# Optimization experiments

Hardware: AMD Instinct MI355X
Metric: run time of the kernel (lower is better)

The kernel has to match this reference:

```python
import jax, jax.numpy as jnp
import numpy as np

B, NN, K, F = 256, 90, 10, 90  # graphs, nodes/graph, retain_node, node_len
TENDENCY = 0.7


def setup_inputs() -> dict:
    key = jax.random.key(0)
    ks = jax.random.split(key, 16)
    N = B * NN
    # fully-connected (no self-loop) edge list per graph, block-offset per graph
    a = np.repeat(np.arange(NN), NN)
    b = np.tile(np.arange(NN), NN)
    m = a != b
    src0, dst0 = a[m], b[m]                      # [8010]
    off = (np.arange(B) * NN)[:, None]
    src = (src0[None, :] + off).ravel()
    dst = (dst0[None, :] + off).ravel()
    edge_index = jnp.asarray(np.stack([src, dst]), dtype=jnp.int64)
    E = edge_index.shape[1]
    batch = jnp.asarray(np.repeat(np.arange(B), NN), dtype=jnp.int64)
    s = 1.0 / np.sqrt(F)
    return {
        "x": jax.random.normal(ks[0], (N, F), jnp.float32),
        "edge_index": edge_index,
        "edge_attr": jax.random.uniform(ks[1], (E,), jnp.float32),
        "batch": batch,
        "W1r": jax.random.normal(ks[2], (F, F), jnp.float32) * s,
        "W1m": jax.random.normal(ks[3], (F, F), jnp.float32) * s,
        "b1": jnp.zeros((F,), jnp.float32),
        "W2r": jax.random.normal(ks[4], (F, F), jnp.float32) * s,
        "W2m": jax.random.normal(ks[5], (F, F), jnp.float32) * s,
        "b2": jnp.zeros((F,), jnp.float32),
        "pool_p": jax.random.normal(ks[6], (F,), jnp.float32),
        "lin_W": jax.random.normal(ks[7], (K * F, 2 * K * F + 1), jnp.float32) / np.sqrt(K * F),
        "lin_b": jnp.zeros((2 * K * F + 1,), jnp.float32),
        "cls_W": jax.random.normal(ks[8], (2 * K * F + 1, 1), jnp.float32) / np.sqrt(2 * K * F + 1),
        "cls_b": jnp.zeros((1,), jnp.float32),
    }


def reference(x, edge_index, edge_attr, batch, W1r, W1m, b1, W2r, W2m, b2,
              pool_p, lin_W, lin_b, cls_W, cls_b):
    src, dst = edge_index[0], edge_index[1]
    N = x.shape[0]

    def conv(h, Wr, Wm, b):  # edge-conditioned message passing
        msg = (h[src] @ Wm) * edge_attr[:, None]          # [E, F]
        agg = jax.ops.segment_sum(msg, dst, num_segments=N)
        return jax.nn.relu(h @ Wr + agg + b)

    def bn(h):  # fresh BatchNorm1d (gamma=1, beta=0), training-mode batch stats
        mu = h.mean(axis=0)
        var = h.var(axis=0)
        return (h - mu) * jax.lax.rsqrt(var + 1e-5)

    x = bn(conv(x, W1r, W1m, b1))
    x = bn(conv(x, W2r, W2m, b2))

    # category-aware top-k pooling: projection score, keep K nodes per graph
    score = TENDENCY * jnp.tanh((x @ pool_p) / jnp.linalg.norm(pool_p))  # [N]
    vals, idx = jax.lax.top_k(score.reshape(B, NN), K)                   # [B, K]
    xb = x.reshape(B, NN, F)
    xs = jnp.take_along_axis(xb, idx[:, :, None], axis=1) * vals[:, :, None]
    perm = (idx + (jnp.arange(B) * NN)[:, None]).reshape(-1)             # global node ids

    h = xs.reshape(B, K * F)
    h = h @ lin_W + lin_b
    out = jax.nn.sigmoid((h @ cls_W + cls_b).reshape(-1))                # [B]
    return (out, perm)
```

## Files before the change

kernel.cpp:

```cpp
#include <hip/hip_runtime.h>
#include <math.h>

#define NG   90
#define PD   96
#define STRD 100
#define KK   10
#define NB   256
#define NTOT (NB*NG)
#define EPG  8010
#define ARR  (PD*STRD)
#define SM_FLOATS (4*ARR)

__global__ __launch_bounds__(512, 2)
void layer_kernel(const float* __restrict__ xin,
                  const float* __restrict__ psIn, int apply_bn,
                  const float* __restrict__ attr,
                  const float* __restrict__ Wm, const float* __restrict__ Wr,
                  const float* __restrict__ bias,
                  float* __restrict__ hout, float* __restrict__ psOut,
                  int do_prep,
                  const float* __restrict__ linW, const float* __restrict__ linb,
                  const float* __restrict__ clsW, const float* __restrict__ clsb,
                  const float* __restrict__ poolp,
                  float* __restrict__ vlin, float* __restrict__ scal)
{
    extern __shared__ float sm[];
    float* s0  = sm;
    float* sA  = s0 + ARR;
    float* sWm = sA + ARR;
    float* sWr = sWm + ARR;
    __shared__ float sSum[96], sSq[96], sMu[96], sRs[96], sStat[192];

    const int g = blockIdx.x, tid = threadIdx.x;
    const int lane = tid & 63, wave = tid >> 6;
    const int cg = tid & 15;
    const int rg = tid >> 4;
    const int r0 = rg * 3;

    if (apply_bn) {
        if (tid < 192) {
            float s = 0.f;
            const float* p = psIn + tid;
#pragma unroll 8
            for (int b = 0; b < NB; b++) s += p[b * 192];
            sStat[tid] = s;
        }
        __syncthreads();
        if (tid < 96) {
            float m = sStat[tid] * (1.f / NTOT);
            float v = sStat[96 + tid] * (1.f / NTOT) - m * m;
            sMu[tid] = m; sRs[tid] = rsqrtf(v + 1e-5f);
        }
    } else if (tid < 96) { sMu[tid] = 0.f; sRs[tid] = 1.f; }
    if (tid < 96) { sSum[tid] = 0.f; sSq[tid] = 0.f; }
    __syncthreads();

    for (int idx = tid; idx < PD * PD; idx += 512) {
        int r = idx / PD, k = idx - (idx / PD) * PD;
        float v = 0.f;
        if (r < NG && k < NG) v = (xin[(size_t)(g * NG + r) * NG + k] - sMu[k]) * sRs[k];
        s0[r * STRD + k] = v;
    }
    for (int idx = tid; idx < PD * PD; idx += 512) {
        int s = idx / PD, d = idx - (idx / PD) * PD;
        float v = 0.f;
        if (s < NG && d < NG && d != s) v = attr[(size_t)g * EPG + s * 89 + (d > s ? d - 1 : d)];
        sA[d * STRD + s] = v;
    }
    for (int idx = tid; idx < PD * PD; idx += 512) {
        int k = idx / PD, c = idx - (idx / PD) * PD;
        bool ok = (k < NG && c < NG);
        sWm[c * STRD + k] = ok ? Wm[k * NG + c] : 0.f;
        sWr[c * STRD + k] = ok ? Wr[k * NG + c] : 0.f;
    }
    __syncthreads();

    float accM[3][6], accR[3][6];
#pragma unroll
    for (int i = 0; i < 3; i++)
#pragma unroll
        for (int j = 0; j < 6; j++) { accM[i][j] = 0.f; accR[i][j] = 0.f; }
    {
        const float* pX = s0 + r0 * STRD;
#pragma unroll 2
        for (int k = 0; k < PD; k += 4) {
            float4 xv[3], wm[6], wr[6];
#pragma unroll
            for (int i = 0; i < 3; i++) xv[i] = *(const float4*)(pX + i * STRD + k);
#pragma unroll
            for (int j = 0; j < 6; j++) {
                const int c = cg + 16 * j;
                wm[j] = *(const float4*)(sWm + c * STRD + k);
                wr[j] = *(const float4*)(sWr + c * STRD + k);
            }
#pragma unroll
            for (int i = 0; i < 3; i++)
#pragma unroll
                for (int j = 0; j < 6; j++) {
                    accM[i][j] = fmaf(xv[i].x, wm[j].x, accM[i][j]);
                    accM[i][j] = fmaf(xv[i].y, wm[j].y, accM[i][j]);
                    accM[i][j] = fmaf(xv[i].z, wm[j].z, accM[i][j]);
                    accM[i][j] = fmaf(xv[i].w, wm[j].w, accM[i][j]);
                    accR[i][j] = fmaf(xv[i].x, wr[j].x, accR[i][j]);
                    accR[i][j] = fmaf(xv[i].y, wr[j].y, accR[i][j]);
                    accR[i][j] = fmaf(xv[i].z, wr[j].z, accR[i][j]);
                    accR[i][j] = fmaf(xv[i].w, wr[j].w, accR[i][j]);
                }
        }
    }
    __syncthreads();

#pragma unroll
    for (int j = 0; j < 6; j++)
#pragma unroll
        for (int i = 0; i < 3; i++)
            s0[(cg + 16 * j) * STRD + (r0 + i)] = accM[i][j];
    __syncthreads();

    float h[3][6];
#pragma unroll
    for (int j = 0; j < 6; j++) {
        const int c = cg + 16 * j;
        float bj = (c < NG) ? bias[c] : 0.f;
#pragma unroll
        for (int i = 0; i < 3; i++) h[i][j] = accR[i][j] + bj;
    }
    {
        const float* pA = sA + r0 * STRD;
#pragma unroll 2
        for (int k = 0; k < PD; k += 4) {
            float4 av[3], mv[6];
#pragma unroll
            for (int i = 0; i < 3; i++) av[i] = *(const float4*)(pA + i * STRD + k);
#pragma unroll
            for (int j = 0; j < 6; j++) mv[j] = *(const float4*)(s0 + (cg + 16 * j) * STRD + k);
#pragma unroll
            for (int i = 0; i < 3; i++)
#pragma unroll
                for (int j = 0; j < 6; j++) {
                    h[i][j] = fmaf(av[i].x, mv[j].x, h[i][j]);
                    h[i][j] = fmaf(av[i].y, mv[j].y, h[i][j]);
                    h[i][j] = fmaf(av[i].z, mv[j].z, h[i][j]);
                    h[i][j] = fmaf(av[i].w, mv[j].w, h[i][j]);
                }
        }
    }

    float cs[6], cq[6];
#pragma unroll
    for (int j = 0; j < 6; j++) { cs[j] = 0.f; cq[j] = 0.f; }
#pragma unroll
    for (int i = 0; i < 3; i++) {
        int r = r0 + i;
        if (r < NG) {
#pragma unroll
            for (int j = 0; j < 6; j++) {
                int c = cg + 16 * j;
                if (c < NG) {
                    float v = fmaxf(h[i][j], 0.f);
                    hout[(size_t)(g * NG + r) * NG + c] = v;
                    cs[j] += v; cq[j] += v * v;
                }
            }
        }
    }
#pragma unroll
    for (int m = 16; m < 64; m <<= 1) {
#pragma unroll
        for (int j = 0; j < 6; j++) {
            cs[j] += __shfl_xor(cs[j], m);
            cq[j] += __shfl_xor(cq[j], m);
        }
    }
    if ((lane >> 4) == 0) {
#pragma unroll
        for (int j = 0; j < 6; j++) {
            int c = cg + 16 * j;
            if (c < NG) { atomicAdd(&sSum[c], cs[j]); atomicAdd(&sSq[c], cq[j]); }
        }
    }
    __syncthreads();
    if (tid < 96) psOut[g * 192 + tid] = sSum[tid];
    else if (tid < 192) psOut[g * 192 + tid] = sSq[tid - 96];

    if (do_prep) {
        if (wave < 4) {
            int row = g + 256 * wave;
            if (row < 900) {
                const float* rw = linW + (size_t)row * 1801;
                float acc = 0.f;
                for (int c2 = lane; c2 < 1801; c2 += 64) acc += rw[c2] * clsW[c2];
                for (int off = 32; off; off >>= 1) acc += __shfl_down(acc, off);
                if (lane == 0) vlin[row] = acc;
            }
        } else if (g == 0 && wave == 4) {
            float acc = 0.f;
            for (int c2 = lane; c2 < 1801; c2 += 64) acc += linb[c2] * clsW[c2];
            for (int off = 32; off; off >>= 1) acc += __shfl_down(acc, off);
            if (lane == 0) scal[0] = acc + clsb[0];
        } else if (g == 0 && wave == 5) {
            float acc = 0.f;
            for (int c2 = lane; c2 < NG; c2 += 64) acc += poolp[c2] * poolp[c2];
            for (int off = 32; off; off >>= 1) acc += __shfl_down(acc, off);
            if (lane == 0) scal[1] = rsqrtf(acc);
        }
    }
}

__global__ __launch_bounds__(256)
void final_kernel(const float* __restrict__ h2, const float* __restrict__ psIn,
                  const float* __restrict__ poolp,
                  const float* __restrict__ vlin, const float* __restrict__ scal,
                  float* __restrict__ out)
{
    __shared__ float sXN[NG * 91];
    __shared__ float sMu[96], sRs[96], sP[96], sStat[192];
    __shared__ float sScore[NG];
    __shared__ int   sIdx[KK];
    __shared__ float sVal[KK];
    __shared__ float sRed[4];
    const int g = blockIdx.x, tid = threadIdx.x;

    if (tid < 192) {
        float s = 0.f;
        const float* p = psIn + tid;
#pragma unroll 8
        for (int b = 0; b < NB; b++) s += p[b * 192];
        sStat[tid] = s;
    }
    __syncthreads();
    if (tid < NG) {
        float m = sStat[tid] * (1.f / NTOT);
        float v = sStat[96 + tid] * (1.f / NTOT) - m * m;
        sMu[tid] = m; sRs[tid] = rsqrtf(v + 1e-5f);
        sP[tid] = poolp[tid];
    }
    __syncthreads();

    const float* hg = h2 + (size_t)g * (NG * NG);
    for (int idx = tid; idx < NG * NG; idx += 256) {
        int d = idx / NG, f = idx - (idx / NG) * NG;
        sXN[d * 91 + f] = (hg[idx] - sMu[f]) * sRs[f];
    }
    __syncthreads();

    if (tid < NG) {
        float s = 0.f;
        for (int f = 0; f < NG; f++) s += sXN[tid * 91 + f] * sP[f];
        sScore[tid] = 0.7f * tanhf(s * scal[1]);
    }
    __syncthreads();

    if (tid < 64) {
        float va = sScore[tid];
        float vb = (tid + 64 < NG) ? sScore[tid + 64] : -1e30f;
        int ia = tid, ib = tid + 64;
        for (int k = 0; k < KK; k++) {
            float v; int i;
            if (va >= vb) { v = va; i = ia; } else { v = vb; i = ib; }
            for (int off = 1; off < 64; off <<= 1) {
                float v2 = __shfl_xor(v, off);
                int   i2 = __shfl_xor(i, off);
                if (v2 > v || (v2 == v && i2 < i)) { v = v2; i = i2; }
            }
            if (tid == 0) { sIdx[k] = i; sVal[k] = v; }
            if (i == ia) va = -1e30f;
            if (i == ib) vb = -1e30f;
        }
    }
    __syncthreads();

    if (tid < KK) out[NB + g * KK + tid] = (float)(g * NG + sIdx[tid]);

    float acc = 0.f;
    for (int j = tid; j < KK * NG; j += 256) {
        int k = j / NG, f = j - (j / NG) * NG;
        acc += sXN[sIdx[k] * 91 + f] * sVal[k] * vlin[j];
    }
    for (int off = 32; off; off >>= 1) acc += __shfl_down(acc, off);
    if ((tid & 63) == 0) sRed[tid >> 6] = acc;
    __syncthreads();
    if (tid == 0) {
        float tot = sRed[0] + sRed[1] + sRed[2] + sRed[3] + scal[0];
        out[g] = 1.f / (1.f + expf(-tot));
    }
}

extern "C" void kernel_launch(void* const* d_in, const int* in_sizes, int n_in,
                              void* d_out, int out_size, void* d_ws, size_t ws_size,
                              hipStream_t stream) {
    const float* x    = (const float*)d_in[0];
    const float* attr = (const float*)d_in[2];
    const float* W1r  = (const float*)d_in[4];
    const float* W1m  = (const float*)d_in[5];
    const float* b1   = (const float*)d_in[6];
    const float* W2r  = (const float*)d_in[7];
    const float* W2m  = (const float*)d_in[8];
    const float* b2   = (const float*)d_in[9];
    const float* poolp= (const float*)d_in[10];
    const float* linW = (const float*)d_in[11];
    const float* linb = (const float*)d_in[12];
    const float* clsW = (const float*)d_in[13];
    const float* clsb = (const float*)d_in[14];

    float* ws   = (float*)d_ws;
    float* ps1  = ws;
    float* ps2  = ps1 + NB * 192;
    float* vlin = ps2 + NB * 192;
    float* scal = vlin + 900;
    float* h1   = scal + 62;
    float* h2   = h1 + (size_t)NTOT * NG;

    const size_t smem = SM_FLOATS * sizeof(float);
    hipFuncSetAttribute((const void*)layer_kernel, hipFuncAttributeMaxDynamicSharedMemorySize, (int)smem);

    layer_kernel<<<NB, 512, smem, stream>>>(x,  nullptr, 0, attr, W1m, W1r, b1, h1, ps1,
                                            1, linW, linb, clsW, clsb, poolp, vlin, scal);
    layer_kernel<<<NB, 512, smem, stream>>>(h1, ps1, 1, attr, W2m, W2r, b2, h2, ps2,
                                            0, linW, linb, clsW, clsb, poolp, vlin, scal);
    final_kernel<<<NB, 256, 0, stream>>>(h2, ps2, poolp, vlin, scal, (float*)d_out);
}
```

Baseline: 234.4 us.

## Double threads per block with 3x3 register tiles and double-buffered LDS loads

Launches the layer kernel with 1024 threads per block instead of 512. Each thread now computes a 3x3 output tile, with waves arranged in a 4x4 grid over the 96x96 padded matrix, instead of a 3x6 tile. Both inner matmul loops are rewritten with software double-buffering of float4 shared-memory loads. The intent is more waves to hide latency and lower register pressure per thread. The trade-off is lower arithmetic intensity per LDS load, since each thread reuses fewer loaded values, plus a tighter launch-bounds register budget.

```diff
diff --git a/kernel.cpp b/kernel.cpp
--- a/kernel.cpp
+++ b/kernel.cpp
@@ -11,7 +11,7 @@
 #define ARR  (PD*STRD)
 #define SM_FLOATS (4*ARR)
 
-__global__ __launch_bounds__(512, 2)
+__global__ __launch_bounds__(1024, 4)
 void layer_kernel(const float* __restrict__ xin,
                   const float* __restrict__ psIn, int apply_bn,
                   const float* __restrict__ attr,
@@ -33,9 +33,9 @@
 
     const int g = blockIdx.x, tid = threadIdx.x;
     const int lane = tid & 63, wave = tid >> 6;
-    const int cg = tid & 15;
-    const int rg = tid >> 4;
-    const int r0 = rg * 3;
+    const int lr = lane >> 3, lc = lane & 7;
+    const int r0 = (wave >> 2) * 24 + lr * 3;
+    const int c0 = (wave & 3) * 24 + lc * 3;
 
     if (apply_bn) {
         if (tid < 192) {
@@ -55,19 +55,19 @@
     if (tid < 96) { sSum[tid] = 0.f; sSq[tid] = 0.f; }
     __syncthreads();
 
-    for (int idx = tid; idx < PD * PD; idx += 512) {
+    for (int idx = tid; idx < PD * PD; idx += 1024) {
         int r = idx / PD, k = idx - (idx / PD) * PD;
         float v = 0.f;
         if (r < NG && k < NG) v = (xin[(size_t)(g * NG + r) * NG + k] - sMu[k]) * sRs[k];
         s0[r * STRD + k] = v;
     }
-    for (int idx = tid; idx < PD * PD; idx += 512) {
+    for (int idx = tid; idx < PD * PD; idx += 1024) {
         int s = idx / PD, d = idx - (idx / PD) * PD;
         float v = 0.f;
         if (s < NG && d < NG && d != s) v = attr[(size_t)g * EPG + s * 89 + (d > s ? d - 1 : d)];
         sA[d * STRD + s] = v;
     }
-    for (int idx = tid; idx < PD * PD; idx += 512) {
+    for (int idx = tid; idx < PD * PD; idx += 1024) {
         int k = idx / PD, c = idx - (idx / PD) * PD;
         bool ok = (k < NG && c < NG);
         sWm[c * STRD + k] = ok ? Wm[k * NG + c] : 0.f;
@@ -75,87 +75,172 @@
     }
     __syncthreads();
 
-    float accM[3][6], accR[3][6];
-#pragma unroll
-    for (int i = 0; i < 3; i++)
-#pragma unroll
-        for (int j = 0; j < 6; j++) { accM[i][j] = 0.f; accR[i][j] = 0.f; }
+    float accM[3][3] = {{0.f,0.f,0.f},{0.f,0.f,0.f},{0.f,0.f,0.f}};
+    float accR[3][3] = {{0.f,0.f,0.f},{0.f,0.f,0.f},{0.f,0.f,0.f}};
     {
-        const float* pX = s0 + r0 * STRD;
+        const float* pX = s0  + r0 * STRD;
+        const float* pm = sWm + c0 * STRD;
+        const float* pr = sWr + c0 * STRD;
+        float4 xa[3], ma[3], ra[3], xb[3], mb[3], rb[3];
+#pragma unroll
+        for (int i = 0; i < 3; i++) {
+            xa[i] = *(const float4*)(pX + i * STRD);
+            ma[i] = *(const float4*)(pm + i * STRD);
+            ra[i] = *(const float4*)(pr + i * STRD);
+        }
 #pragma unroll 2
-        for (int k = 0; k < PD; k += 4) {
-            float4 xv[3], wm[6], wr[6];
-#pragma unroll
-            for (int i = 0; i < 3; i++) xv[i] = *(const float4*)(pX + i * STRD + k);
-#pragma unroll
-            for (int j = 0; j < 6; j++) {
-                const int c = cg + 16 * j;
-                wm[j] = *(const float4*)(sWm + c * STRD + k);
-                wr[j] = *(const float4*)(sWr + c * STRD + k);
+        for (int k = 0; k < 88; k += 8) {
+#pragma unroll
+            for (int i = 0; i < 3; i++) {
+                xb[i] = *(const float4*)(pX + i * STRD + k + 4);
+                mb[i] = *(const float4*)(pm + i * STRD + k + 4);
+                rb[i] = *(const float4*)(pr + i * STRD + k + 4);
             }
 #pragma unroll
             for (int i = 0; i < 3; i++)
 #pragma unroll
-                for (int j = 0; j < 6; j++) {
-                    accM[i][j] = fmaf(xv[i].x, wm[j].x, accM[i][j]);
-                    accM[i][j] = fmaf(xv[i].y, wm[j].y, accM[i][j]);
-                    accM[i][j] = fmaf(xv[i].z, wm[j].z, accM[i][j]);
-                    accM[i][j] = fmaf(xv[i].w, wm[j].w, accM[i][j]);
-                    accR[i][j] = fmaf(xv[i].x, wr[j].x, accR[i][j]);
-                    accR[i][j] = fmaf(xv[i].y, wr[j].y, accR[i][j]);
-                    accR[i][j] = fmaf(xv[i].z, wr[j].z, accR[i][j]);
-                    accR[i][j] = fmaf(xv[i].w, wr[j].w, accR[i][j]);
+                for (int j = 0; j < 3; j++) {
+                    accM[i][j] = fmaf(xa[i].x, ma[j].x, accM[i][j]);
+                    accM[i][j] = fmaf(xa[i].y, ma[j].y, accM[i][j]);
+                    accM[i][j] = fmaf(xa[i].z, ma[j].z, accM[i][j]);
+                    accM[i][j] = fmaf(xa[i].w, ma[j].w, accM[i][j]);
+                    accR[i][j] = fmaf(xa[i].x, ra[j].x, accR[i][j]);
+                    accR[i][j] = fmaf(xa[i].y, ra[j].y, accR[i][j]);
+                    accR[i][j] = fmaf(xa[i].z, ra[j].z, accR[i][j]);
+                    accR[i][j] = fmaf(xa[i].w, ra[j].w, accR[i][j]);
                 }
-        }
-    }
-    __syncthreads();
-
-#pragma unroll
-    for (int j = 0; j < 6; j++)
+#pragma unroll
+            for (int i = 0; i < 3; i++) {
+                xa[i] = *(const float4*)(pX + i * STRD + k + 8);
+                ma[i] = *(const float4*)(pm + i * STRD + k + 8);
+                ra[i] = *(const float4*)(pr + i * STRD + k + 8);
+            }
+#pragma unroll
+            for (int i = 0; i < 3; i++)
+#pragma unroll
+                for (int j = 0; j < 3; j++) {
+                    accM[i][j] = fmaf(xb[i].x, mb[j].x, accM[i][j]);
+                    accM[i][j] = fmaf(xb[i].y, mb[j].y, accM[i][j]);
+                    accM[i][j] = fmaf(xb[i].z, mb[j].z, accM[i][j]);
+                    accM[i][j] = fmaf(xb[i].w, mb[j].w, accM[i][j]);
+                    accR[i][j] = fmaf(xb[i].x, rb[j].x, accR[i][j]);
+                    accR[i][j] = fmaf(xb[i].y, rb[j].y, accR[i][j]);
+                    accR[i][j] = fmaf(xb[i].z, rb[j].z, accR[i][j]);
+                    accR[i][j] = fmaf(xb[i].w, rb[j].w, accR[i][j]);
+                }
+        }
+#pragma unroll
+        for (int i = 0; i < 3; i++) {
+            xb[i] = *(const float4*)(pX + i * STRD + 92);
+            mb[i] = *(const float4*)(pm + i * STRD + 92);
+            rb[i] = *(const float4*)(pr + i * STRD + 92);
+        }
 #pragma unroll
         for (int i = 0; i < 3; i++)
-            s0[(cg + 16 * j) * STRD + (r0 + i)] = accM[i][j];
-    __syncthreads();
-
-    float h[3][6];
-#pragma unroll
-    for (int j = 0; j < 6; j++) {
-        const int c = cg + 16 * j;
-        float bj = (c < NG) ? bias[c] : 0.f;
+#pragma unroll
+            for (int j = 0; j < 3; j++) {
+                accM[i][j] = fmaf(xa[i].x, ma[j].x, accM[i][j]);
+                accM[i][j] = fmaf(xa[i].y, ma[j].y, accM[i][j]);
+                accM[i][j] = fmaf(xa[i].z, ma[j].z, accM[i][j]);
+                accM[i][j] = fmaf(xa[i].w, ma[j].w, accM[i][j]);
+                accR[i][j] = fmaf(xa[i].x, ra[j].x, accR[i][j]);
+                accR[i][j] = fmaf(xa[i].y, ra[j].y, accR[i][j]);
+                accR[i][j] = fmaf(xa[i].z, ra[j].z, accR[i][j]);
+                accR[i][j] = fmaf(xa[i].w, ra[j].w, accR[i][j]);
+                accM[i][j] = fmaf(xb[i].x, mb[j].x, accM[i][j]);
+                accM[i][j] = fmaf(xb[i].y, mb[j].y, accM[i][j]);
+                accM[i][j] = fmaf(xb[i].z, mb[j].z, accM[i][j]);
+                accM[i][j] = fmaf(xb[i].w, mb[j].w, accM[i][j]);
+                accR[i][j] = fmaf(xb[i].x, rb[j].x, accR[i][j]);
+                accR[i][j] = fmaf(xb[i].y, rb[j].y, accR[i][j]);
+                accR[i][j] = fmaf(xb[i].z, rb[j].z, accR[i][j]);
+                accR[i][j] = fmaf(xb[i].w, rb[j].w, accR[i][j]);
+            }
+    }
+    __syncthreads();
+
+#pragma unroll
+    for (int j = 0; j < 3; j++)
+#pragma unroll
+        for (int i = 0; i < 3; i++)
+            s0[(c0 + j) * STRD + (r0 + i)] = accM[i][j];
+    __syncthreads();
+
+    float h[3][3];
+#pragma unroll
+    for (int j = 0; j < 3; j++) {
+        float bj = (c0 + j < NG) ? bias[c0 + j] : 0.f;
 #pragma unroll
         for (int i = 0; i < 3; i++) h[i][j] = accR[i][j] + bj;
     }
     {
         const float* pA = sA + r0 * STRD;
+        const float* pM = s0 + c0 * STRD;
+        float4 aa[3], sa[3], ab[3], sb[3];
+#pragma unroll
+        for (int i = 0; i < 3; i++) {
+            aa[i] = *(const float4*)(pA + i * STRD);
+            sa[i] = *(const float4*)(pM + i * STRD);
+        }
 #pragma unroll 2
-        for (int k = 0; k < PD; k += 4) {
-            float4 av[3], mv[6];
-#pragma unroll
-            for (int i = 0; i < 3; i++) av[i] = *(const float4*)(pA + i * STRD + k);
-#pragma unroll
-            for (int j = 0; j < 6; j++) mv[j] = *(const float4*)(s0 + (cg + 16 * j) * STRD + k);
+        for (int k = 0; k < 88; k += 8) {
+#pragma unroll
+            for (int i = 0; i < 3; i++) {
+                ab[i] = *(const float4*)(pA + i * STRD + k + 4);
+                sb[i] = *(const float4*)(pM + i * STRD + k + 4);
+            }
 #pragma unroll
             for (int i = 0; i < 3; i++)
 #pragma unroll
-                for (int j = 0; j < 6; j++) {
-                    h[i][j] = fmaf(av[i].x, mv[j].x, h[i][j]);
-                    h[i][j] = fmaf(av[i].y, mv[j].y, h[i][j]);
-                    h[i][j] = fmaf(av[i].z, mv[j].z, h[i][j]);
-                    h[i][j] = fmaf(av[i].w, mv[j].w, h[i][j]);
+                for (int j = 0; j < 3; j++) {
+                    h[i][j] = fmaf(aa[i].x, sa[j].x, h[i][j]);
+                    h[i][j] = fmaf(aa[i].y, sa[j].y, h[i][j]);
+                    h[i][j] = fmaf(aa[i].z, sa[j].z, h[i][j]);
+                    h[i][j] = fmaf(aa[i].w, sa[j].w, h[i][j]);
                 }
-        }
-    }
-
-    float cs[6], cq[6];
-#pragma unroll
-    for (int j = 0; j < 6; j++) { cs[j] = 0.f; cq[j] = 0.f; }
+#pragma unroll
+            for (int i = 0; i < 3; i++) {
+                aa[i] = *(const float4*)(pA + i * STRD + k + 8);
+                sa[i] = *(const float4*)(pM + i * STRD + k + 8);
+            }
+#pragma unroll
+            for (int i = 0; i < 3; i++)
+#pragma unroll
+                for (int j = 0; j < 3; j++) {
+                    h[i][j] = fmaf(ab[i].x, sb[j].x, h[i][j]);
+                    h[i][j] = fmaf(ab[i].y, sb[j].y, h[i][j]);
+                    h[i][j] = fmaf(ab[i].z, sb[j].z, h[i][j]);
+                    h[i][j] = fmaf(ab[i].w, sb[j].w, h[i][j]);
+                }
+        }
+#pragma unroll
+        for (int i = 0; i < 3; i++) {
+            ab[i] = *(const float4*)(pA + i * STRD + 92);
+            sb[i] = *(const float4*)(pM + i * STRD + 92);
+        }
+#pragma unroll
+        for (int i = 0; i < 3; i++)
+#pragma unroll
+            for (int j = 0; j < 3; j++) {
+                h[i][j] = fmaf(aa[i].x, sa[j].x, h[i][j]);
+                h[i][j] = fmaf(aa[i].y, sa[j].y, h[i][j]);
+                h[i][j] = fmaf(aa[i].z, sa[j].z, h[i][j]);
+                h[i][j] = fmaf(aa[i].w, sa[j].w, h[i][j]);
+                h[i][j] = fmaf(ab[i].x, sb[j].x, h[i][j]);
+                h[i][j] = fmaf(ab[i].y, sb[j].y, h[i][j]);
+                h[i][j] = fmaf(ab[i].z, sb[j].z, h[i][j]);
+                h[i][j] = fmaf(ab[i].w, sb[j].w, h[i][j]);
+            }
+    }
+
+    float cs[3] = {0.f,0.f,0.f}, cq[3] = {0.f,0.f,0.f};
 #pragma unroll
     for (int i = 0; i < 3; i++) {
         int r = r0 + i;
         if (r < NG) {
 #pragma unroll
-            for (int j = 0; j < 6; j++) {
-                int c = cg + 16 * j;
+            for (int j = 0; j < 3; j++) {
+                int c = c0 + j;
                 if (c < NG) {
                     float v = fmaxf(h[i][j], 0.f);
                     hout[(size_t)(g * NG + r) * NG + c] = v;
@@ -165,17 +250,17 @@
         }
     }
 #pragma unroll
-    for (int m = 16; m < 64; m <<= 1) {
-#pragma unroll
-        for (int j = 0; j < 6; j++) {
+    for (int m = 8; m < 64; m <<= 1) {
+#pragma unroll
+        for (int j = 0; j < 3; j++) {
             cs[j] += __shfl_xor(cs[j], m);
             cq[j] += __shfl_xor(cq[j], m);
         }
     }
-    if ((lane >> 4) == 0) {
-#pragma unroll
-        for (int j = 0; j < 6; j++) {
-            int c = cg + 16 * j;
+    if (lr == 0) {
+#pragma unroll
+        for (int j = 0; j < 3; j++) {
+            int c = c0 + j;
             if (c < NG) { atomicAdd(&sSum[c], cs[j]); atomicAdd(&sSq[c], cq[j]); }
         }
     }
@@ -314,9 +399,9 @@
     const size_t smem = SM_FLOATS * sizeof(float);
     hipFuncSetAttribute((const void*)layer_kernel, hipFuncAttributeMaxDynamicSharedMemorySize, (int)smem);
 
-    layer_kernel<<<NB, 512, smem, stream>>>(x,  nullptr, 0, attr, W1m, W1r, b1, h1, ps1,
-                                            1, linW, linb, clsW, clsb, poolp, vlin, scal);
-    layer_kernel<<<NB, 512, smem, stream>>>(h1, ps1, 1, attr, W2m, W2r, b2, h2, ps2,
-                                            0, linW, linb, clsW, clsb, poolp, vlin, scal);
+    layer_kernel<<<NB, 1024, smem, stream>>>(x,  nullptr, 0, attr, W1m, W1r, b1, h1, ps1,
+                                             1, linW, linb, clsW, clsb, poolp, vlin, scal);
+    layer_kernel<<<NB, 1024, smem, stream>>>(h1, ps1, 1, attr, W2m, W2r, b2, h2, ps2,
+                                             0, linW, linb, clsW, clsb, poolp, vlin, scal);
     final_kernel<<<NB, 256, 0, stream>>>(h2, ps2, poolp, vlin, scal, (float*)d_out);
 }
```

After: 212.4 us. 1.1x faster.
